# Kernel tuning notes

Measured on AMD Instinct MI355X. Metric: run time of the kernel, lower is better.

The kernel has to match this reference:

```python
import jax, jax.numpy as jnp
import numpy as np

N = 100000
E = 1600000
F_IN = 256
HEADS = 8
C1 = 8
NCLS = 16
NEG_SLOPE = 0.2


def setup_inputs() -> dict:
    key = jax.random.key(0)
    ks = jax.random.split(key, 8)
    x = jax.random.normal(ks[0], (N, F_IN), dtype=jnp.float32)
    edge_index = jax.random.randint(ks[1], (2, E), 0, N, dtype=jnp.int64)
    W1 = jax.random.normal(ks[2], (F_IN, HEADS * C1), dtype=jnp.float32) * (1.0 / np.sqrt(F_IN))
    a1_src = jax.random.normal(ks[3], (HEADS, C1), dtype=jnp.float32) * 0.1
    a1_dst = jax.random.normal(ks[4], (HEADS, C1), dtype=jnp.float32) * 0.1
    b1 = jnp.zeros((HEADS * C1,), dtype=jnp.float32)
    W2 = jax.random.normal(ks[5], (HEADS * C1, NCLS), dtype=jnp.float32) * (1.0 / np.sqrt(HEADS * C1))
    a2_src = jax.random.normal(ks[6], (1, NCLS), dtype=jnp.float32) * 0.1
    a2_dst = jax.random.normal(ks[7], (1, NCLS), dtype=jnp.float32) * 0.1
    b2 = jnp.zeros((NCLS,), dtype=jnp.float32)
    return {"x": x, "edge_index": edge_index, "W1": W1, "a1_src": a1_src,
            "a1_dst": a1_dst, "b1": b1, "W2": W2, "a2_src": a2_src,
            "a2_dst": a2_dst, "b2": b2}


def gat_layer(x, src, dst, W, a_src, a_dst, b, heads, out_c, concat):
    n = x.shape[0]
    h = (x @ W).reshape(n, heads, out_c)            # [N,H,C]
    al_src = (h * a_src).sum(-1)                    # [N,H]
    al_dst = (h * a_dst).sum(-1)                    # [N,H]
    e = jax.nn.leaky_relu(al_src[src] + al_dst[dst], NEG_SLOPE)  # [E',H]
    m = jax.ops.segment_max(e, dst, num_segments=n)              # per-dst max
    alpha = jnp.exp(e - m[dst])
    denom = jax.ops.segment_sum(alpha, dst, num_segments=n)
    alpha = alpha / denom[dst]
    out = jax.ops.segment_sum(h[src] * alpha[:, :, None], dst, num_segments=n)  # [N,H,C]
    out = out.reshape(n, heads * out_c) if concat else out.mean(axis=1)
    return out + b


def reference(x, edge_index, W1, a1_src, a1_dst, b1, W2, a2_src, a2_dst, b2):
    # add self-loops (PyG GATConv default)
    loop = jnp.arange(N, dtype=edge_index.dtype)
    src = jnp.concatenate([edge_index[0], loop])
    dst = jnp.concatenate([edge_index[1], loop])
    # dropout layers are identity in eval mode
    h = jax.nn.elu(gat_layer(x, src, dst, W1, a1_src, a1_dst, b1, HEADS, C1, True))
    out = gat_layer(h, src, dst, W2, a2_src, a2_dst, b2, 1, NCLS, False)
    return jax.nn.log_softmax(out, axis=-1)
```

## Files before the change

### kernel.cpp

```cpp
#include <hip/hip_runtime.h>
#include <math.h>

#define NN   100000
#define EE   1600000
#define FIN  256
#define NCLS 16
#define NEG  0.2f

#define NEDGE (EE + NN)
#define WBKT  256
#define NBKT  ((NN + WBKT - 1) / WBKT)
#define CAP   5120
#define ABLK  4096
#define NABLK ((NEDGE + ABLK - 1) / ABLK)
#define NGBLK ((NN + 63) / 64)

#define OFF_GCNT  0
#define OFF_BASE  392
#define OFF_ROW   784
#define OFF_BKT   100788
#define OFF_ADJ   (OFF_BKT + NBKT*CAP)
#define OFF_H1B   (OFF_ADJ + NEDGE)
#define OFF_H1E   (OFF_H1B + NN*32)
#define OFF_AL1S  (OFF_H1E + NN*32)
#define OFF_AL1D  (OFF_AL1S + NN*8)
#define OFF_H2B   (OFF_AL1D + NN*8)
#define OFF_AL2S  (OFF_H2B + NN*8)
#define OFF_AL2D  (OFF_AL2S + NN)

__device__ __forceinline__ float lrelu(float x) { return x >= 0.f ? x : NEG * x; }
__device__ __forceinline__ unsigned short f2bf(float x) {
    unsigned u = __float_as_uint(x);
    return (unsigned short)((u + 0x7FFF + ((u >> 16) & 1)) >> 16);
}
__device__ __forceinline__ float bf2f(unsigned short b) {
    return __uint_as_float(((unsigned)b) << 16);
}
__device__ __forceinline__ float bflo(unsigned u) { return __uint_as_float(u << 16); }
__device__ __forceinline__ float bfhi(unsigned u) { return __uint_as_float(u & 0xFFFF0000u); }


__device__ __forceinline__ void gemm1_body(
    char* smem, int n0, int t,
    const float* __restrict__ x, const float* __restrict__ W1,
    const float* __restrict__ a1s, const float* __restrict__ a1d,
    unsigned short* __restrict__ h1b, float* __restrict__ al1s, float* __restrict__ al1d)
{
    float (*sxT)[68] = (float(*)[68])smem;
    float (*sW)[64]  = (float(*)[64])(smem + 32 * 68 * 4);
    const int tr = t >> 4, tc = t & 15;

    const int xr0 = t >> 3,         xf0 = t & 7;
    const int xr1 = (t + 256) >> 3, xf1 = (t + 256) & 7;
    const int wr0 = t >> 4,         wf0 = t & 15;
    const int wr1 = (t + 256) >> 4, wf1 = (t + 256) & 15;
    const int nx0 = n0 + xr0, nx1 = n0 + xr1;

    float acc[4][4] = {};
    float4 px0, px1, pw0, pw1;

    px0 = (nx0 < NN) ? *(const float4*)(x + (size_t)nx0 * FIN + xf0 * 4)
                     : make_float4(0.f, 0.f, 0.f, 0.f);
    px1 = (nx1 < NN) ? *(const float4*)(x + (size_t)nx1 * FIN + xf1 * 4)
                     : make_float4(0.f, 0.f, 0.f, 0.f);
    pw0 = *(const float4*)(W1 + (size_t)wr0 * 64 + wf0 * 4);
    pw1 = *(const float4*)(W1 + (size_t)wr1 * 64 + wf1 * 4);

    for (int kc = 0; kc < 256; kc += 32) {
        __syncthreads();
        sxT[xf0 * 4 + 0][xr0] = px0.x;
        sxT[xf0 * 4 + 1][xr0] = px0.y;
        sxT[xf0 * 4 + 2][xr0] = px0.z;
        sxT[xf0 * 4 + 3][xr0] = px0.w;
        sxT[xf1 * 4 + 0][xr1] = px1.x;
        sxT[xf1 * 4 + 1][xr1] = px1.y;
        sxT[xf1 * 4 + 2][xr1] = px1.z;
        sxT[xf1 * 4 + 3][xr1] = px1.w;
        *(float4*)&sW[wr0][wf0 * 4] = pw0;
        *(float4*)&sW[wr1][wf1 * 4] = pw1;
        __syncthreads();

        if (kc + 32 < 256) {
            int kn = kc + 32;
            px0 = (nx0 < NN) ? *(const float4*)(x + (size_t)nx0 * FIN + kn + xf0 * 4)
                             : make_float4(0.f, 0.f, 0.f, 0.f);
            px1 = (nx1 < NN) ? *(const float4*)(x + (size_t)nx1 * FIN + kn + xf1 * 4)
                             : make_float4(0.f, 0.f, 0.f, 0.f);
            pw0 = *(const float4*)(W1 + (size_t)(kn + wr0) * 64 + wf0 * 4);
            pw1 = *(const float4*)(W1 + (size_t)(kn + wr1) * 64 + wf1 * 4);
        }

        #pragma unroll
        for (int k = 0; k < 32; ++k) {
            float4 a = *(const float4*)&sxT[k][tr * 4];
            float4 b = *(const float4*)&sW[k][tc * 4];
            acc[0][0] += a.x * b.x; acc[0][1] += a.x * b.y; acc[0][2] += a.x * b.z; acc[0][3] += a.x * b.w;
            acc[1][0] += a.y * b.x; acc[1][1] += a.y * b.y; acc[1][2] += a.y * b.z; acc[1][3] += a.y * b.w;
            acc[2][0] += a.z * b.x; acc[2][1] += a.z * b.y; acc[2][2] += a.z * b.z; acc[2][3] += a.z * b.w;
            acc[3][0] += a.w * b.x; acc[3][1] += a.w * b.y; acc[3][2] += a.w * b.z; acc[3][3] += a.w * b.w;
        }
    }

    #pragma unroll
    for (int j = 0; j < 4; ++j) {
        int n = n0 + tr * 4 + j;
        if (n < NN) {
            ushort4 v = make_ushort4(f2bf(acc[j][0]), f2bf(acc[j][1]), f2bf(acc[j][2]), f2bf(acc[j][3]));
            *(ushort4*)(h1b + (size_t)n * 64 + tc * 4) = v;
        }
    }

    float sa[4], da[4];
    #pragma unroll
    for (int u = 0; u < 4; ++u) { sa[u] = a1s[tc * 4 + u]; da[u] = a1d[tc * 4 + u]; }
    #pragma unroll
    for (int j = 0; j < 4; ++j) {
        float vs = acc[j][0] * sa[0] + acc[j][1] * sa[1] + acc[j][2] * sa[2] + acc[j][3] * sa[3];
        float vd = acc[j][0] * da[0] + acc[j][1] * da[1] + acc[j][2] * da[2] + acc[j][3] * da[3];
        vs += __shfl_xor(vs, 1, 64);
        vd += __shfl_xor(vd, 1, 64);
        int n = n0 + tr * 4 + j;
        if (!(tc & 1) && n < NN) {
            al1s[n * 8 + (tc >> 1)] = vs;
            al1d[n * 8 + (tc >> 1)] = vd;
        }
    }
}

__device__ __forceinline__ void binA_body(
    char* smem, int blk, int t,
    const int* __restrict__ esrc, const int* __restrict__ edst,
    int* __restrict__ gcnt, unsigned* __restrict__ bkt)
{
    int* lcnt  = (int*)smem;
    int* lbase = lcnt + NBKT;
    const int e0 = blk * ABLK;
    for (int i = t; i < NBKT; i += 256) lcnt[i] = 0;
    __syncthreads();

    unsigned wrd[16];
    unsigned short bb[16], ll[16];
    #pragma unroll
    for (int j = 0; j < 16; ++j) {
        int ei = e0 + j * 256 + t;
        bb[j] = 0xFFFFu;
        if (ei < NEDGE) {
            int s, d;
            if (ei < EE) { s = esrc[ei]; d = edst[ei]; } else { s = d = ei - EE; }
            int b = d >> 8;
            wrd[j] = ((unsigned)s << 8) | (unsigned)(d & 255);
            bb[j] = (unsigned short)b;
            ll[j] = (unsigned short)atomicAdd(&lcnt[b], 1);
        }
    }
    __syncthreads();
    for (int i = t; i < NBKT; i += 256)
        lbase[i] = lcnt[i] ? atomicAdd(&gcnt[i], lcnt[i]) : 0;
    __syncthreads();
    #pragma unroll
    for (int j = 0; j < 16; ++j) {
        if (bb[j] != 0xFFFFu) {
            int b = bb[j];
            bkt[(size_t)b * CAP + lbase[b] + ll[j]] = wrd[j];
        }
    }
}

__global__ __launch_bounds__(256) void k_binA_gemm1(
    const int* __restrict__ esrc, const int* __restrict__ edst,
    int* __restrict__ gcnt, unsigned* __restrict__ bkt,
    const float* __restrict__ x, const float* __restrict__ W1,
    const float* __restrict__ a1s, const float* __restrict__ a1d,
    unsigned short* __restrict__ h1b, float* __restrict__ al1s, float* __restrict__ al1d)
{
    __shared__ __align__(16) char smem[16896];
    const int t = threadIdx.x;
    if (blockIdx.x < NABLK)
        binA_body(smem, blockIdx.x, t, esrc, edst, gcnt, bkt);
    else
        gemm1_body(smem, (blockIdx.x - NABLK) * 64, t, x, W1, a1s, a1d, h1b, al1s, al1d);
}

__global__ __launch_bounds__(512) void k_scanB(
    const int* __restrict__ gcnt, int* __restrict__ base, int* __restrict__ row)
{
    __shared__ int s[512];
    int t = threadIdx.x;
    int v = (t < NBKT) ? gcnt[t] : 0;
    s[t] = v;
    __syncthreads();
    for (int off = 1; off < 512; off <<= 1) {
        int u = (t >= off) ? s[t - off] : 0;
        __syncthreads();
        s[t] += u;
        __syncthreads();
    }
    if (t <= NBKT) base[t] = s[t] - v;
    if (t == 0) row[NN] = NEDGE;
}

__global__ __launch_bounds__(256) void k_binC(
    const int* __restrict__ gcnt, const int* __restrict__ base,
    const unsigned* __restrict__ bkt, int* __restrict__ row, int* __restrict__ adj)
{
    __shared__ unsigned wd[CAP];
    __shared__ int hist[256], pref[256], cnt2[256];
    const int g = blockIdx.x, t = threadIdx.x;
    const int cn = gcnt[g], bs = base[g];
    hist[t] = 0; cnt2[t] = 0;
    __syncthreads();
    for (int i = t; i < cn; i += 256) {
        unsigned w = bkt[(size_t)g * CAP + i];
        wd[i] = w;
        atomicAdd(&hist[w & 255], 1);
    }
    __syncthreads();
    int v = hist[t];
    pref[t] = v;
    __syncthreads();
    for (int off = 1; off < 256; off <<= 1) {
        int u = (t >= off) ? pref[t - off] : 0;
        __syncthreads();
        pref[t] += u;
        __syncthreads();
    }
    int ex = pref[t] - v;
    int n = g * 256 + t;
    if (n < NN) row[n] = bs + ex;
    pref[t] = ex;
    __syncthreads();
    for (int i = t; i < cn; i += 256) {
        unsigned w = wd[i];
        int dl = w & 255;
        int p = atomicAdd(&cnt2[dl], 1);
        adj[bs + pref[dl] + p] = (int)(w >> 8);
    }
}

__global__ __launch_bounds__(256) void k_agg1(
    const int* __restrict__ row, const int* __restrict__ adj,
    const float* __restrict__ al1s, const float* __restrict__ al1d,
    const unsigned* __restrict__ h1b2, const float* __restrict__ b1,
    unsigned* __restrict__ h1e2)
{
    const int wv = threadIdx.x >> 6, lane = threadIdx.x & 63;
    const int n = blockIdx.x * 4 + wv;
    const int q = lane >> 4;
    const int r = lane & 15;
    const int h = r >> 1;
    const float ald = al1d[n * 8 + h];
    const int r0 = row[n], r1 = row[n + 1];

    float dsum = 0.f, ax = 0.f, ay = 0.f, bx = 0.f, by = 0.f;
    for (int c0 = r0; c0 < r1; c0 += 64) {
        int li = c0 + lane;
        int adjv = adj[li < r1 ? li : r0];
        int m = r1 - c0; if (m > 64) m = 64;
        int k = 0;
        for (; k + 16 <= m; k += 16) {
            int s0 = __shfl(adjv, k + 0  + q, 64);
            int s1 = __shfl(adjv, k + 4  + q, 64);
            int s2 = __shfl(adjv, k + 8  + q, 64);
            int s3 = __shfl(adjv, k + 12 + q, 64);
            float a0 = al1s[s0 * 8 + h];
            float a1 = al1s[s1 * 8 + h];
            float a2 = al1s[s2 * 8 + h];
            float a3 = al1s[s3 * 8 + h];
            uint2 u0 = *(const uint2*)(h1b2 + s0 * 32 + r * 2);
            uint2 u1 = *(const uint2*)(h1b2 + s1 * 32 + r * 2);
            uint2 u2 = *(const uint2*)(h1b2 + s2 * 32 + r * 2);
            uint2 u3 = *(const uint2*)(h1b2 + s3 * 32 + r * 2);
            float w0 = __expf(lrelu(a0 + ald));
            float w1 = __expf(lrelu(a1 + ald));
            float w2 = __expf(lrelu(a2 + ald));
            float w3 = __expf(lrelu(a3 + ald));
            dsum += (w0 + w1) + (w2 + w3);
            ax += w0 * bflo(u0.x) + w1 * bflo(u1.x) + w2 * bflo(u2.x) + w3 * bflo(u3.x);
            ay += w0 * bfhi(u0.x) + w1 * bfhi(u1.x) + w2 * bfhi(u2.x) + w3 * bfhi(u3.x);
            bx += w0 * bflo(u0.y) + w1 * bflo(u1.y) + w2 * bflo(u2.y) + w3 * bflo(u3.y);
            by += w0 * bfhi(u0.y) + w1 * bfhi(u1.y) + w2 * bfhi(u2.y) + w3 * bfhi(u3.y);
        }
        for (; k < m; k += 4) {
            int kk = k + q;
            bool act = kk < m;
            int s0 = __shfl(adjv, act ? kk : 0, 64);
            float w0 = act ? __expf(lrelu(al1s[s0 * 8 + h] + ald)) : 0.f;
            uint2 u0 = *(const uint2*)(h1b2 + s0 * 32 + r * 2);
            dsum += w0;
            ax += w0 * bflo(u0.x);
            ay += w0 * bfhi(u0.x);
            bx += w0 * bflo(u0.y);
            by += w0 * bfhi(u0.y);
        }
    }
    dsum += __shfl_xor(dsum, 16, 64); dsum += __shfl_xor(dsum, 32, 64);
    ax   += __shfl_xor(ax,   16, 64); ax   += __shfl_xor(ax,   32, 64);
    ay   += __shfl_xor(ay,   16, 64); ay   += __shfl_xor(ay,   32, 64);
    bx   += __shfl_xor(bx,   16, 64); bx   += __shfl_xor(bx,   32, 64);
    by   += __shfl_xor(by,   16, 64); by   += __shfl_xor(by,   32, 64);

    float inv = 1.f / dsum;
    float v0 = ax * inv + b1[r * 4 + 0];
    float v1 = ay * inv + b1[r * 4 + 1];
    float v2 = bx * inv + b1[r * 4 + 2];
    float v3 = by * inv + b1[r * 4 + 3];
    v0 = v0 > 0.f ? v0 : __expf(v0) - 1.f;
    v1 = v1 > 0.f ? v1 : __expf(v1) - 1.f;
    v2 = v2 > 0.f ? v2 : __expf(v2) - 1.f;
    v3 = v3 > 0.f ? v3 : __expf(v3) - 1.f;
    if (q == 0) {
        uint2 o;
        o.x = (unsigned)f2bf(v0) | ((unsigned)f2bf(v1) << 16);
        o.y = (unsigned)f2bf(v2) | ((unsigned)f2bf(v3) << 16);
        *(uint2*)(h1e2 + n * 32 + r * 2) = o;
    }
}

__global__ __launch_bounds__(256) void k_gemm2(
    const unsigned* __restrict__ h1e2, const float* __restrict__ W2,
    const float* __restrict__ a2s, const float* __restrict__ a2d,
    unsigned short* __restrict__ h2b, float* __restrict__ al2s, float* __restrict__ al2d)
{
    __shared__ float sW[64 * 16];
    __shared__ unsigned sh[16][33];
    const int t = threadIdx.x;
    for (int i = t; i < 64 * 16; i += 256) sW[i] = W2[i];
    const int nb = blockIdx.x * 16;
    {
        int idx = t * 2;
        int rrow = idx >> 5, rcol = idx & 31;
        uint2 v = *(const uint2*)(h1e2 + (size_t)(nb + rrow) * 32 + rcol);
        sh[rrow][rcol]     = v.x;
        sh[rrow][rcol + 1] = v.y;
    }
    __syncthreads();
    const int ln = t >> 4;
    const int k  = t & 15;
    const int n  = nb + ln;
    float acc = 0.f;
    #pragma unroll
    for (int c2 = 0; c2 < 32; ++c2) {
        unsigned u = sh[ln][c2];
        acc += bflo(u) * sW[(c2 * 2) * 16 + k] + bfhi(u) * sW[(c2 * 2 + 1) * 16 + k];
    }
    h2b[(size_t)n * 16 + k] = f2bf(acc);
    float vs = acc * a2s[k], vd = acc * a2d[k];
    #pragma unroll
    for (int off = 1; off < 16; off <<= 1) {
        vs += __shfl_xor(vs, off, 64);
        vd += __shfl_xor(vd, off, 64);
    }
    if (k == 0) { al2s[n] = vs; al2d[n] = vd; }
}

__global__ __launch_bounds__(256) void k_agg2(
    const int* __restrict__ row, const int* __restrict__ adj,
    const float* __restrict__ al2s, const float* __restrict__ al2d,
    const unsigned* __restrict__ h2b2, const float* __restrict__ b2,
    float* __restrict__ out)
{
    const int wv = threadIdx.x >> 6, lane = threadIdx.x & 63;
    const int n = blockIdx.x * 4 + wv;
    const float ald = al2d[n];
    const int r0 = row[n], r1 = row[n + 1];

    const int j = lane >> 2;
    const int r = lane & 3;
    float dsum = 0.f, ax = 0.f, ay = 0.f, bx = 0.f, by = 0.f;
    for (int i = r0; i < r1; i += 16) {
        int i0 = i + j;
        bool act = i0 < r1;
        int s = adj[act ? i0 : r0];
        float w = act ? __expf(lrelu(al2s[s] + ald)) : 0.f;
        uint2 u = *(const uint2*)(h2b2 + s * 8 + r * 2);
        dsum += w;
        ax += w * bflo(u.x);
        ay += w * bfhi(u.x);
        bx += w * bflo(u.y);
        by += w * bfhi(u.y);
    }
    #pragma unroll
    for (int off = 4; off < 64; off <<= 1) {
        dsum += __shfl_xor(dsum, off, 64);
        ax   += __shfl_xor(ax,   off, 64);
        ay   += __shfl_xor(ay,   off, 64);
        bx   += __shfl_xor(bx,   off, 64);
        by   += __shfl_xor(by,   off, 64);
    }
    float inv = 1.f / dsum;
    float v0 = ax * inv + b2[r * 4 + 0];
    float v1 = ay * inv + b2[r * 4 + 1];
    float v2 = bx * inv + b2[r * 4 + 2];
    float v3 = by * inv + b2[r * 4 + 3];

    float mx = fmaxf(fmaxf(v0, v1), fmaxf(v2, v3));
    mx = fmaxf(mx, __shfl_xor(mx, 1, 64));
    mx = fmaxf(mx, __shfl_xor(mx, 2, 64));
    float se = __expf(v0 - mx) + __expf(v1 - mx) + __expf(v2 - mx) + __expf(v3 - mx);
    se += __shfl_xor(se, 1, 64);
    se += __shfl_xor(se, 2, 64);
    float ls = mx + __logf(se);
    if (j == 0)
        *(float4*)(out + (size_t)n * 16 + r * 4) = make_float4(v0 - ls, v1 - ls, v2 - ls, v3 - ls);
}

extern "C" void kernel_launch(void* const* d_in, const int* in_sizes, int n_in,
                              void* d_out, int out_size, void* d_ws, size_t ws_size,
                              hipStream_t stream)
{
    const float* x    = (const float*)d_in[0];
    const int*   eidx = (const int*)d_in[1];
    const float* W1   = (const float*)d_in[2];
    const float* a1s  = (const float*)d_in[3];
    const float* a1d  = (const float*)d_in[4];
    const float* b1   = (const float*)d_in[5];
    const float* W2   = (const float*)d_in[6];
    const float* a2s  = (const float*)d_in[7];
    const float* a2d  = (const float*)d_in[8];
    const float* b2   = (const float*)d_in[9];
    float* out = (float*)d_out;
    float* ws  = (float*)d_ws;

    const int* esrc = eidx;
    const int* edst = eidx + EE;

    int* gcnt = (int*)(ws + OFF_GCNT);
    int* base = (int*)(ws + OFF_BASE);
    int* row  = (int*)(ws + OFF_ROW);
    unsigned* bkt = (unsigned*)(ws + OFF_BKT);
    int* adj  = (int*)(ws + OFF_ADJ);
    unsigned short* h1b = (unsigned short*)(ws + OFF_H1B);
    unsigned short* h1e = (unsigned short*)(ws + OFF_H1E);
    float* al1s  = ws + OFF_AL1S;
    float* al1d  = ws + OFF_AL1D;
    unsigned short* h2b = (unsigned short*)(ws + OFF_H2B);
    float* al2s  = ws + OFF_AL2S;
    float* al2d  = ws + OFF_AL2D;

    hipMemsetAsync(gcnt, 0, 392 * sizeof(int), stream);

    k_binA_gemm1<<<NABLK + NGBLK, 256, 0, stream>>>(esrc, edst, gcnt, bkt,
                                                    x, W1, a1s, a1d, h1b, al1s, al1d);
    k_scanB<<<1,    512, 0, stream>>>(gcnt, base, row);
    k_binC <<<NBKT, 256, 0, stream>>>(gcnt, base, bkt, row, adj);

    k_agg1 <<<NN / 4, 256, 0, stream>>>(row, adj, al1s, al1d, (const unsigned*)h1b, b1, (unsigned*)h1e);
    k_gemm2<<<NN / 16, 256, 0, stream>>>((const unsigned*)h1e, W2, a2s, a2d, h2b, al2s, al2d);
    k_agg2 <<<NN / 4, 256, 0, stream>>>(row, adj, al2s, al2d, (const unsigned*)h2b, b2, out);
}
```

Before: 357.3 us.

## Halve CSR bucket width and fold bucket-offset scan into binning kernel

The single-block k_scanB launch is removed. Each k_binC block now computes its own bucket base by reducing the counts of all preceding buckets, and the last block writes row[NN]. Bucket width drops from 256 to 128 destinations, which doubles the number of buckets and binC blocks, halves shared-memory capacity per block and improves parallelism. The cost is redundant prefix-sum work, up to about 782 loads per block, plus more global atomics in binA because there are more buckets to count.

Result: no change. 355.9 us (-0.4%).

```diff
diff --git a/kernel.cpp b/kernel.cpp
--- a/kernel.cpp
+++ b/kernel.cpp
@@ -8,17 +8,16 @@
 #define NEG  0.2f
 
 #define NEDGE (EE + NN)
-#define WBKT  256
+#define WBKT  128
 #define NBKT  ((NN + WBKT - 1) / WBKT)
-#define CAP   5120
+#define CAP   2560
 #define ABLK  4096
 #define NABLK ((NEDGE + ABLK - 1) / ABLK)
 #define NGBLK ((NN + 63) / 64)
 
 #define OFF_GCNT  0
-#define OFF_BASE  392
-#define OFF_ROW   784
-#define OFF_BKT   100788
+#define OFF_ROW   1024
+#define OFF_BKT   101026
 #define OFF_ADJ   (OFF_BKT + NBKT*CAP)
 #define OFF_H1B   (OFF_ADJ + NEDGE)
 #define OFF_H1E   (OFF_H1B + NN*32)
@@ -147,8 +146,8 @@
         if (ei < NEDGE) {
             int s, d;
             if (ei < EE) { s = esrc[ei]; d = edst[ei]; } else { s = d = ei - EE; }
-            int b = d >> 8;
-            wrd[j] = ((unsigned)s << 8) | (unsigned)(d & 255);
+            int b = d / WBKT;
+            wrd[j] = ((unsigned)s << 8) | (unsigned)(d & (WBKT - 1));
             bb[j] = (unsigned short)b;
             ll[j] = (unsigned short)atomicAdd(&lcnt[b], 1);
         }
@@ -181,57 +180,51 @@
         gemm1_body(smem, (blockIdx.x - NABLK) * 64, t, x, W1, a1s, a1d, h1b, al1s, al1d);
 }
 
-__global__ __launch_bounds__(512) void k_scanB(
-    const int* __restrict__ gcnt, int* __restrict__ base, int* __restrict__ row)
-{
-    __shared__ int s[512];
-    int t = threadIdx.x;
-    int v = (t < NBKT) ? gcnt[t] : 0;
-    s[t] = v;
-    __syncthreads();
-    for (int off = 1; off < 512; off <<= 1) {
-        int u = (t >= off) ? s[t - off] : 0;
+__global__ __launch_bounds__(256) void k_binC(
+    const int* __restrict__ gcnt,
+    const unsigned* __restrict__ bkt, int* __restrict__ row, int* __restrict__ adj)
+{
+    __shared__ unsigned wd[CAP];
+    __shared__ int hist[WBKT], pref[WBKT], cnt2[WBKT];
+    __shared__ int sred[256];
+    const int g = blockIdx.x, t = threadIdx.x;
+    const int cn = gcnt[g];
+    int partial = 0;
+    for (int i = t; i < g; i += 256) partial += gcnt[i];
+    sred[t] = partial;
+    if (t < WBKT) { hist[t] = 0; cnt2[t] = 0; }
+    __syncthreads();
+    #pragma unroll
+    for (int off = 128; off > 0; off >>= 1) {
+        if (t < off) sred[t] += sred[t + off];
         __syncthreads();
-        s[t] += u;
-        __syncthreads();
-    }
-    if (t <= NBKT) base[t] = s[t] - v;
-    if (t == 0) row[NN] = NEDGE;
-}
-
-__global__ __launch_bounds__(256) void k_binC(
-    const int* __restrict__ gcnt, const int* __restrict__ base,
-    const unsigned* __restrict__ bkt, int* __restrict__ row, int* __restrict__ adj)
-{
-    __shared__ unsigned wd[CAP];
-    __shared__ int hist[256], pref[256], cnt2[256];
-    const int g = blockIdx.x, t = threadIdx.x;
-    const int cn = gcnt[g], bs = base[g];
-    hist[t] = 0; cnt2[t] = 0;
-    __syncthreads();
+    }
+    const int bs = sred[0];
+
     for (int i = t; i < cn; i += 256) {
         unsigned w = bkt[(size_t)g * CAP + i];
         wd[i] = w;
-        atomicAdd(&hist[w & 255], 1);
-    }
-    __syncthreads();
-    int v = hist[t];
-    pref[t] = v;
-    __syncthreads();
-    for (int off = 1; off < 256; off <<= 1) {
-        int u = (t >= off) ? pref[t - off] : 0;
+        atomicAdd(&hist[w & (WBKT - 1)], 1);
+    }
+    __syncthreads();
+    int v = (t < WBKT) ? hist[t] : 0;
+    if (t < WBKT) pref[t] = v;
+    __syncthreads();
+    for (int off = 1; off < WBKT; off <<= 1) {
+        int u = (t >= off && t < WBKT) ? pref[t - off] : 0;
         __syncthreads();
-        pref[t] += u;
+        if (t < WBKT) pref[t] += u;
         __syncthreads();
     }
-    int ex = pref[t] - v;
-    int n = g * 256 + t;
-    if (n < NN) row[n] = bs + ex;
-    pref[t] = ex;
+    int ex = pref[(t < WBKT) ? t : 0] - v;
+    int n = g * WBKT + t;
+    if (t < WBKT && n < NN) row[n] = bs + ex;
+    if (t < WBKT) pref[t] = ex;
+    if (g == NBKT - 1 && t == 0) row[NN] = NEDGE;
     __syncthreads();
     for (int i = t; i < cn; i += 256) {
         unsigned w = wd[i];
-        int dl = w & 255;
+        int dl = w & (WBKT - 1);
         int p = atomicAdd(&cnt2[dl], 1);
         adj[bs + pref[dl] + p] = (int)(w >> 8);
     }
@@ -425,7 +418,6 @@
     const int* edst = eidx + EE;
 
     int* gcnt = (int*)(ws + OFF_GCNT);
-    int* base = (int*)(ws + OFF_BASE);
     int* row  = (int*)(ws + OFF_ROW);
     unsigned* bkt = (unsigned*)(ws + OFF_BKT);
     int* adj  = (int*)(ws + OFF_ADJ);
@@ -437,12 +429,11 @@
     float* al2s  = ws + OFF_AL2S;
     float* al2d  = ws + OFF_AL2D;
 
-    hipMemsetAsync(gcnt, 0, 392 * sizeof(int), stream);
+    hipMemsetAsync(gcnt, 0, NBKT * sizeof(int), stream);
 
     k_binA_gemm1<<<NABLK + NGBLK, 256, 0, stream>>>(esrc, edst, gcnt, bkt,
                                                     x, W1, a1s, a1d, h1b, al1s, al1d);
-    k_scanB<<<1,    512, 0, stream>>>(gcnt, base, row);
-    k_binC <<<NBKT, 256, 0, stream>>>(gcnt, base, bkt, row, adj);
+    k_binC <<<NBKT, 256, 0, stream>>>(gcnt, bkt, row, adj);
 
     k_agg1 <<<NN / 4, 256, 0, stream>>>(row, adj, al1s, al1d, (const unsigned*)h1b, b1, (unsigned*)h1e);
     k_gemm2<<<NN / 16, 256, 0, stream>>>((const unsigned*)h1e, W2, a2s, a2d, h2b, al2s, al2d);
```
